# Optimization experiments

Hardware: AMD Instinct MI355X
Metric: run time of the kernel (lower is better)

Reference implementation:

```python
import jax, jax.numpy as jnp
import numpy as np

TEMPERATURE = 0.07
NUM_HARD_NEGATIVES = 5
BATCH, DIM = 4096, 768


def setup_inputs() -> dict:
    key = jax.random.key(0)
    k1, k2 = jax.random.split(key)
    return {
        "text_emb": jax.random.normal(k1, (BATCH, DIM), dtype=jnp.float32),
        "table_emb": jax.random.normal(k2, (BATCH, DIM), dtype=jnp.float32),
    }


def _ttcl_loss(text_emb, table_emb):
    # F.normalize(dim=1)
    t = text_emb / jnp.linalg.norm(text_emb, axis=1, keepdims=True)
    z = table_emb / jnp.linalg.norm(table_emb, axis=1, keepdims=True)
    sim = z @ t.T  # [B, B], sim[i, j] = <table_i, text_j>
    B = sim.shape[0]
    pos = jnp.diagonal(sim) / TEMPERATURE  # [B], <text_i, table_i> == <table_i, text_i>
    diag_mask = jnp.eye(B, dtype=bool)
    neg_inf = jnp.finfo(sim.dtype).min

    def hard_neg_loss(neg_rows):
        # neg_rows[i] holds the B candidate negatives for sample i; exclude self.
        neg = jnp.where(diag_mask, neg_inf, neg_rows)
        top_vals, _ = jax.lax.top_k(neg, NUM_HARD_NEGATIVES)  # [B, k]
        logits = jnp.concatenate([pos[:, None], top_vals / TEMPERATURE], axis=1)  # [B, k+1]
        # cross_entropy with label 0 == -log_softmax(logits)[:, 0]
        return -jax.nn.log_softmax(logits, axis=1)[:, 0]

    # t2z: negatives for i are sim[j][i], j != i  -> column i -> rows of sim.T
    loss_t2z = jnp.sum(hard_neg_loss(sim.T))
    # z2t: negatives for i are sim[i][j], j != i  -> row i
    loss_z2t = jnp.sum(hard_neg_loss(sim))
    loss = (loss_t2z + loss_z2t) / (2 * B)
    return loss, sim


def reference(text_emb, table_emb):
    return _ttcl_loss(text_emb, table_emb)
```

## Files before the change

### kernel.cpp

```cpp
#include <hip/hip_runtime.h>
#include <stdint.h>
#include <math.h>

#define BSZ 4096
#define DIM 768
#define TEMP 0.07f

typedef short short8 __attribute__((ext_vector_type(8)));
typedef float f32x4 __attribute__((ext_vector_type(4)));


__device__ __forceinline__ uint16_t f2bf(float f) {
  uint32_t u = __float_as_uint(f);
  uint32_t r = (u + 0x7FFFu + ((u >> 16) & 1u)) >> 16;
  return (uint16_t)r;
}

__device__ __forceinline__ void gll16(const void* g, void* l) {
  __builtin_amdgcn_global_load_lds(
      (__attribute__((address_space(1))) void*)(uintptr_t)g,
      (__attribute__((address_space(3))) void*)l,
      16, 0, 0);
}

__device__ __forceinline__ void ins5(float v, float& a, float& b, float& c,
                                     float& d, float& e) {
  if (v > e) {
    e = v;
    if (e > d) { float t = d; d = e; e = t;
      if (d > c) { t = c; c = d; d = t;
        if (c > b) { t = b; b = c; c = t;
          if (b > a) { t = a; a = b; b = t; } } } }
  }
}

__device__ __forceinline__ void sins5(float v, float& a, float& b, float& c,
                                      float& d, float& e) {
  float t;
  t = fmaxf(a, v); v = fminf(a, v); a = t;
  t = fmaxf(b, v); v = fminf(b, v); b = t;
  t = fmaxf(c, v); v = fminf(c, v); c = t;
  t = fmaxf(d, v); v = fminf(d, v); d = t;
  e = fmaxf(e, v);
}

__global__ __launch_bounds__(256) void k_norm(const float* __restrict__ text,
                                              const float* __restrict__ table,
                                              uint16_t* __restrict__ tn,
                                              uint16_t* __restrict__ zn) {
  int row = blockIdx.x & (BSZ - 1);
  bool isTable = blockIdx.x >= BSZ;
  const float* src = (isTable ? table : text) + (size_t)row * DIM;
  uint16_t* dst = (isTable ? zn : tn) + (size_t)row * DIM;
  int tid = threadIdx.x;

  float x0 = src[tid];
  float x1 = src[tid + 256];
  float x2 = src[tid + 512];
  float ss = x0 * x0 + x1 * x1 + x2 * x2;
  #pragma unroll
  for (int off = 32; off >= 1; off >>= 1) ss += __shfl_xor(ss, off);
  __shared__ float wss[4];
  if ((tid & 63) == 0) wss[tid >> 6] = ss;
  __syncthreads();
  float inv = rsqrtf(wss[0] + wss[1] + wss[2] + wss[3]);
  dst[tid]       = f2bf(x0 * inv);
  dst[tid + 256] = f2bf(x1 * inv);
  dst[tid + 512] = f2bf(x2 * inv);
}

__global__ __launch_bounds__(512, 2) void k_gemm(const uint16_t* __restrict__ Zb,
                                                 const uint16_t* __restrict__ Tb,
                                                 float* __restrict__ sim) {
  extern __shared__ __attribute__((aligned(16))) char lds[];

  int tid = threadIdx.x;
  int wave = tid >> 6, lane = tid & 63;
  int wm = wave >> 2, wn = wave & 3;
  int brow = (blockIdx.x >> 4) << 8;
  int bcol = (blockIdx.x & 15) << 8;

  f32x4 acc[8][4] = {};

  const uint16_t* gA = Zb + (size_t)brow * DIM;
  const uint16_t* gB = Tb + (size_t)bcol * DIM;

  int r7 = lane & 7;
  int kqg = lane >> 4;
  int rlo = lane & 15;

  int srow = (wave << 5) + (lane >> 3);
  int sc = ((lane & 7) ^ (srow & 7)) << 3;

  auto SA = [&](int t, int bb, int j) {
    gll16(gA + (size_t)(srow + j * 8) * DIM + t * 64 + sc,
          lds + bb + (wave << 12) + (j << 10));
  };
  auto SB = [&](int t, int bb, int j) {
    gll16(gB + (size_t)(srow + j * 8) * DIM + t * 64 + sc,
          lds + bb + 32768 + (wave << 12) + (j << 10));
  };

  auto LOADB = [&](int bb, short8 (&bf)[2][4]) {
    const char* Bb = lds + bb + 32768;
    #pragma unroll
    for (int ks = 0; ks < 2; ++ks) {
      int ch = (((ks << 2) + kqg) ^ r7) << 4;
      #pragma unroll
      for (int n = 0; n < 4; ++n) {
        int R = (wn << 6) + (n << 4) + rlo;
        bf[ks][n] = *(const short8*)(Bb + (R << 7) + ch);
      }
    }
  };
  auto PHASE = [&](int bb, int mlo, short8 (&bf)[2][4]) {
    __builtin_amdgcn_s_setprio(1);
    #pragma unroll
    for (int ks = 0; ks < 2; ++ks) {
      int ch = (((ks << 2) + kqg) ^ r7) << 4;
      #pragma unroll
      for (int mm = 0; mm < 4; ++mm) {
        int R = (wm << 7) + ((mlo + mm) << 4) + rlo;
        short8 af = *(const short8*)(lds + bb + (R << 7) + ch);
        #pragma unroll
        for (int n = 0; n < 4; ++n)
          acc[mlo + mm][n] = __builtin_amdgcn_mfma_f32_16x16x32_bf16(
              af, bf[ks][n], acc[mlo + mm][n], 0, 0, 0);
      }
    }
    __builtin_amdgcn_s_setprio(0);
  };

  #pragma unroll
  for (int j = 0; j < 4; ++j) { SA(0, 0, j); SB(0, 0, j); }
  #pragma unroll
  for (int j = 0; j < 4; ++j) { SA(1, 65536, j); SB(1, 65536, j); }
  asm volatile("s_waitcnt vmcnt(8)" ::: "memory");
  __builtin_amdgcn_s_barrier();

  #pragma unroll 2
  for (int t = 0; t < 10; ++t) {
    int bb = (t & 1) << 16;
    short8 bf[2][4];
    LOADB(bb, bf);
    PHASE(bb, 0, bf);
    __builtin_amdgcn_s_barrier();
    if ((wave & 2) == 0) {
      SA(t + 2, bb, 0); SA(t + 2, bb, 1); SA(t + 2, bb, 2); SA(t + 2, bb, 3);
    }
    SB(t + 2, bb, 0); SB(t + 2, bb, 1);
    SB(t + 2, bb, 2); SB(t + 2, bb, 3);
    PHASE(bb, 4, bf);
    __builtin_amdgcn_s_barrier();
    if ((wave & 2) != 0) {
      SA(t + 2, bb, 0); SA(t + 2, bb, 1); SA(t + 2, bb, 2); SA(t + 2, bb, 3);
    }
    asm volatile("s_waitcnt vmcnt(8)" ::: "memory");
    __builtin_amdgcn_s_barrier();
  }

  {
    short8 bf[2][4];
    LOADB(0, bf);
    PHASE(0, 0, bf);
    PHASE(0, 4, bf);
  }
  asm volatile("s_waitcnt vmcnt(0)" ::: "memory");
  __builtin_amdgcn_s_barrier();
  {
    short8 bf[2][4];
    LOADB(65536, bf);
    PHASE(65536, 0, bf);
    PHASE(65536, 4, bf);
  }

  int crow0 = brow + (wm << 7) + ((lane >> 4) << 2);
  int ccol0 = bcol + (wn << 6) + (lane & 15);
  #pragma unroll
  for (int m = 0; m < 8; ++m)
    #pragma unroll
    for (int n = 0; n < 4; ++n)
      #pragma unroll
      for (int r = 0; r < 4; ++r)
        sim[(size_t)(crow0 + m * 16 + r) * BSZ + (ccol0 + n * 16)] = acc[m][n][r];
}

__global__ __launch_bounds__(256) void k_tile(const float* __restrict__ sim,
                                              float* __restrict__ rp,
                                              float* __restrict__ cp) {
  extern __shared__ float l32[];
  int tid = threadIdx.x;
  int tr = blockIdx.x >> 5, tc = blockIdx.x & 31;
  int row0 = tr << 7, col0 = tc << 7;
  bool diag = (tr == tc);

  int q = tid & 31;
  int g = tid >> 5;
  const float* gsrc = sim + (size_t)(row0 + (g << 4)) * BSZ + col0 + (q << 2);

  f32x4 v[16];
  #pragma unroll
  for (int k = 0; k < 16; ++k)
    v[k] = *(const f32x4*)(gsrc + (size_t)k * BSZ);

  #pragma unroll
  for (int k = 0; k < 16; ++k) {
    int r = (g << 4) + k;
    if (diag && (r >> 2) == q) v[k][r & 3] = -1e30f;
    *(f32x4*)(l32 + (r << 7) + ((q ^ (r & 7)) << 2)) = v[k];
  }
  __syncthreads();

  {
    int row = tid >> 1, h = tid & 1;
    int rx = row & 7;
    const float* rb = l32 + (row << 7);
    float a0 = -1e30f, a1 = -1e30f, a2 = -1e30f, a3 = -1e30f, a4 = -1e30f;
    #pragma unroll
    for (int j = 0; j < 16; ++j) {
      int c16 = (h << 4) + j;
      f32x4 x = *(const f32x4*)(rb + ((c16 ^ rx) << 2));
      sins5(x[0], a0, a1, a2, a3, a4);
      sins5(x[1], a0, a1, a2, a3, a4);
      sins5(x[2], a0, a1, a2, a3, a4);
      sins5(x[3], a0, a1, a2, a3, a4);
    }
    float b0 = __shfl_xor(a0, 1), b1 = __shfl_xor(a1, 1),
          b2 = __shfl_xor(a2, 1), b3 = __shfl_xor(a3, 1),
          b4 = __shfl_xor(a4, 1);
    sins5(b0, a0, a1, a2, a3, a4);
    sins5(b1, a0, a1, a2, a3, a4);
    sins5(b2, a0, a1, a2, a3, a4);
    sins5(b3, a0, a1, a2, a3, a4);
    sins5(b4, a0, a1, a2, a3, a4);
    if (h == 0) {
      float* pr = rp + ((size_t)(row0 + row) * 32 + tc) * 5;
      pr[0] = a0; pr[1] = a1; pr[2] = a2; pr[3] = a3; pr[4] = a4;
    }
  }

  {
    int c = tid >> 1, hf = tid & 1;
    int cc = c >> 2, cw = c & 3;
    float a0 = -1e30f, a1 = -1e30f, a2 = -1e30f, a3 = -1e30f, a4 = -1e30f;
    #pragma unroll 8
    for (int k = 0; k < 64; ++k) {
      int r = (hf << 6) + k;
      float x = l32[(r << 7) + (((cc ^ (r & 7)) << 2) | cw)];
      sins5(x, a0, a1, a2, a3, a4);
    }
    float b0 = __shfl_xor(a0, 1), b1 = __shfl_xor(a1, 1),
          b2 = __shfl_xor(a2, 1), b3 = __shfl_xor(a3, 1),
          b4 = __shfl_xor(a4, 1);
    sins5(b0, a0, a1, a2, a3, a4);
    sins5(b1, a0, a1, a2, a3, a4);
    sins5(b2, a0, a1, a2, a3, a4);
    sins5(b3, a0, a1, a2, a3, a4);
    sins5(b4, a0, a1, a2, a3, a4);
    if (hf == 0) {
      float* pc = cp + ((size_t)(col0 + c) * 32 + tr) * 5;
      pc[0] = a0; pc[1] = a1; pc[2] = a2; pc[3] = a3; pc[4] = a4;
    }
  }
}

__global__ __launch_bounds__(256) void k_merge(const float* __restrict__ sim,
                                               const float* __restrict__ rp,
                                               const float* __restrict__ cp,
                                               float* __restrict__ lossbuf) {
  int wave = threadIdx.x >> 6, lane = threadIdx.x & 63;
  int wid = blockIdx.x * 4 + wave;
  bool isCol = wid >= BSZ;
  int line = isCol ? wid - BSZ : wid;
  const float* src = (isCol ? cp : rp) + (size_t)line * 160;

  float t0 = -1e30f, t1 = -1e30f, t2 = -1e30f, t3 = -1e30f, t4 = -1e30f;
  ins5(src[lane], t0, t1, t2, t3, t4);
  ins5(src[lane + 64], t0, t1, t2, t3, t4);
  if (lane < 32) ins5(src[lane + 128], t0, t1, t2, t3, t4);

  float top[5];
  #pragma unroll
  for (int e = 0; e < 5; e++) {
    float m = t0;
    #pragma unroll
    for (int off = 32; off >= 1; off >>= 1) m = fmaxf(m, __shfl_xor(m, off));
    unsigned long long msk = __ballot(t0 == m);
    int owner = __ffsll(msk) - 1;
    if (lane == owner) { t0 = t1; t1 = t2; t2 = t3; t3 = t4; t4 = -1e30f; }
    top[e] = m;
  }

  if (lane == 0) {
    float pos = sim[(size_t)line * BSZ + line] / TEMP;
    float l0 = top[0] / TEMP, l1 = top[1] / TEMP, l2 = top[2] / TEMP,
          l3 = top[3] / TEMP, l4 = top[4] / TEMP;
    float mx = fmaxf(pos, fmaxf(fmaxf(l0, l1), fmaxf(fmaxf(l2, l3), l4)));
    float s = expf(pos - mx) + expf(l0 - mx) + expf(l1 - mx) +
              expf(l2 - mx) + expf(l3 - mx) + expf(l4 - mx);
    lossbuf[wid] = mx + logf(s) - pos;
  }
}

__global__ __launch_bounds__(256) void k_reduce(const float* __restrict__ losses,
                                                float* __restrict__ out) {
  int tid = threadIdx.x;
  float s = 0.f;
  for (int i = tid; i < 2 * BSZ; i += 256) s += losses[i];
  #pragma unroll
  for (int off = 32; off >= 1; off >>= 1) s += __shfl_xor(s, off);
  __shared__ float wss[4];
  if ((tid & 63) == 0) wss[tid >> 6] = s;
  __syncthreads();
  if (tid == 0) out[0] = (wss[0] + wss[1] + wss[2] + wss[3]) / (2.0f * BSZ);
}

extern "C" void kernel_launch(void* const* d_in, const int* in_sizes, int n_in,
                              void* d_out, int out_size, void* d_ws, size_t ws_size,
                              hipStream_t stream) {
  const float* text = (const float*)d_in[0];
  const float* table = (const float*)d_in[1];
  float* out = (float*)d_out;
  float* sim = out + 1;

  uint16_t* Zb = (uint16_t*)d_ws;
  uint16_t* Tb = Zb + (size_t)BSZ * DIM;
  float* lossbuf = (float*)(Tb + (size_t)BSZ * DIM);

  float* rp = (float*)d_ws;
  float* cp = rp + (size_t)BSZ * 32 * 5;

  k_norm<<<2 * BSZ, 256, 0, stream>>>(text, table, Tb, Zb);
  k_gemm<<<(BSZ / 256) * (BSZ / 256), 512, 131072, stream>>>(Zb, Tb, sim);
  k_tile<<<32 * 32, 256, 65536, stream>>>(sim, rp, cp);
  k_merge<<<2 * BSZ / 4, 256, 0, stream>>>(sim, rp, cp, lossbuf);
  k_reduce<<<1, 256, 0, stream>>>(lossbuf, out);
}
```

Baseline: 84.36 us.

## Vectorize norm kernel and halve top-k tile height with XCD-aware block mapping

The norm kernel now uses 192 threads, each doing one float4 load and one packed 4-bf16 store instead of three scalar accesses. The top-k tile kernel switches to 64x128 tiles with half the shared memory, giving twice as many blocks. Block indices are remapped so that neighbouring column tiles land on the same XCD. Column partials now hold 64 per-tile top-5 entries per column, so the merge kernel reads 320 values on the column path. The aim is better occupancy and cache locality, in exchange for more partial data to merge.

```diff
diff --git a/kernel.cpp b/kernel.cpp
--- a/kernel.cpp
+++ b/kernel.cpp
@@ -7,6 +7,7 @@
 #define TEMP 0.07f
 
 typedef short short8 __attribute__((ext_vector_type(8)));
+typedef short short4v __attribute__((ext_vector_type(4)));
 typedef float f32x4 __attribute__((ext_vector_type(4)));
 
 
@@ -44,7 +45,7 @@
   e = fmaxf(e, v);
 }
 
-__global__ __launch_bounds__(256) void k_norm(const float* __restrict__ text,
+__global__ __launch_bounds__(192) void k_norm(const float* __restrict__ text,
                                               const float* __restrict__ table,
                                               uint16_t* __restrict__ tn,
                                               uint16_t* __restrict__ zn) {
@@ -54,19 +55,20 @@
   uint16_t* dst = (isTable ? zn : tn) + (size_t)row * DIM;
   int tid = threadIdx.x;
 
-  float x0 = src[tid];
-  float x1 = src[tid + 256];
-  float x2 = src[tid + 512];
-  float ss = x0 * x0 + x1 * x1 + x2 * x2;
+  f32x4 v = *(const f32x4*)(src + tid * 4);
+  float ss = v[0] * v[0] + v[1] * v[1] + v[2] * v[2] + v[3] * v[3];
   #pragma unroll
   for (int off = 32; off >= 1; off >>= 1) ss += __shfl_xor(ss, off);
-  __shared__ float wss[4];
+  __shared__ float wss[3];
   if ((tid & 63) == 0) wss[tid >> 6] = ss;
   __syncthreads();
-  float inv = rsqrtf(wss[0] + wss[1] + wss[2] + wss[3]);
-  dst[tid]       = f2bf(x0 * inv);
-  dst[tid + 256] = f2bf(x1 * inv);
-  dst[tid + 512] = f2bf(x2 * inv);
+  float inv = rsqrtf(wss[0] + wss[1] + wss[2]);
+  short4v o;
+  o[0] = (short)f2bf(v[0] * inv);
+  o[1] = (short)f2bf(v[1] * inv);
+  o[2] = (short)f2bf(v[2] * inv);
+  o[3] = (short)f2bf(v[3] * inv);
+  *(short4v*)(dst + tid * 4) = o;
 }
 
 __global__ __launch_bounds__(512, 2) void k_gemm(const uint16_t* __restrict__ Zb,
@@ -190,49 +192,57 @@
                                               float* __restrict__ cp) {
   extern __shared__ float l32[];
   int tid = threadIdx.x;
-  int tr = blockIdx.x >> 5, tc = blockIdx.x & 31;
-  int row0 = tr << 7, col0 = tc << 7;
-  bool diag = (tr == tc);
+
+  int xcd = blockIdx.x & 7, li = blockIdx.x >> 3;
+  int tc = (xcd << 1) + (li & 1) + (((li >> 1) & 1) << 4);
+  int tr = li >> 2;
+  int row0 = tr << 6, col0 = tc << 7;
+  bool diag = ((tr >> 1) == tc);
+  int lcbase = (tr & 1) << 6;
 
   int q = tid & 31;
   int g = tid >> 5;
-  const float* gsrc = sim + (size_t)(row0 + (g << 4)) * BSZ + col0 + (q << 2);
-
-  f32x4 v[16];
-  #pragma unroll
-  for (int k = 0; k < 16; ++k)
+  const float* gsrc = sim + (size_t)(row0 + (g << 3)) * BSZ + col0 + (q << 2);
+
+  f32x4 v[8];
+  #pragma unroll
+  for (int k = 0; k < 8; ++k)
     v[k] = *(const f32x4*)(gsrc + (size_t)k * BSZ);
 
   #pragma unroll
-  for (int k = 0; k < 16; ++k) {
-    int r = (g << 4) + k;
-    if (diag && (r >> 2) == q) v[k][r & 3] = -1e30f;
+  for (int k = 0; k < 8; ++k) {
+    int r = (g << 3) + k;
+    int lc = lcbase + r;
+    if (diag && (lc >> 2) == q) v[k][lc & 3] = -1e30f;
     *(f32x4*)(l32 + (r << 7) + ((q ^ (r & 7)) << 2)) = v[k];
   }
   __syncthreads();
 
   {
-    int row = tid >> 1, h = tid & 1;
+    int row = tid >> 2, h = tid & 3;
     int rx = row & 7;
     const float* rb = l32 + (row << 7);
     float a0 = -1e30f, a1 = -1e30f, a2 = -1e30f, a3 = -1e30f, a4 = -1e30f;
     #pragma unroll
-    for (int j = 0; j < 16; ++j) {
-      int c16 = (h << 4) + j;
+    for (int j = 0; j < 8; ++j) {
+      int c16 = (h << 3) + j;
       f32x4 x = *(const f32x4*)(rb + ((c16 ^ rx) << 2));
       sins5(x[0], a0, a1, a2, a3, a4);
       sins5(x[1], a0, a1, a2, a3, a4);
       sins5(x[2], a0, a1, a2, a3, a4);
       sins5(x[3], a0, a1, a2, a3, a4);
     }
-    float b0 = __shfl_xor(a0, 1), b1 = __shfl_xor(a1, 1),
-          b2 = __shfl_xor(a2, 1), b3 = __shfl_xor(a3, 1),
-          b4 = __shfl_xor(a4, 1);
-    sins5(b0, a0, a1, a2, a3, a4);
-    sins5(b1, a0, a1, a2, a3, a4);
-    sins5(b2, a0, a1, a2, a3, a4);
-    sins5(b3, a0, a1, a2, a3, a4);
-    sins5(b4, a0, a1, a2, a3, a4);
+    #pragma unroll
+    for (int xr = 1; xr <= 2; xr <<= 1) {
+      float b0 = __shfl_xor(a0, xr), b1 = __shfl_xor(a1, xr),
+            b2 = __shfl_xor(a2, xr), b3 = __shfl_xor(a3, xr),
+            b4 = __shfl_xor(a4, xr);
+      sins5(b0, a0, a1, a2, a3, a4);
+      sins5(b1, a0, a1, a2, a3, a4);
+      sins5(b2, a0, a1, a2, a3, a4);
+      sins5(b3, a0, a1, a2, a3, a4);
+      sins5(b4, a0, a1, a2, a3, a4);
+    }
     if (h == 0) {
       float* pr = rp + ((size_t)(row0 + row) * 32 + tc) * 5;
       pr[0] = a0; pr[1] = a1; pr[2] = a2; pr[3] = a3; pr[4] = a4;
@@ -244,8 +254,8 @@
     int cc = c >> 2, cw = c & 3;
     float a0 = -1e30f, a1 = -1e30f, a2 = -1e30f, a3 = -1e30f, a4 = -1e30f;
     #pragma unroll 8
-    for (int k = 0; k < 64; ++k) {
-      int r = (hf << 6) + k;
+    for (int k = 0; k < 32; ++k) {
+      int r = (hf << 5) + k;
       float x = l32[(r << 7) + (((cc ^ (r & 7)) << 2) | cw)];
       sins5(x, a0, a1, a2, a3, a4);
     }
@@ -258,7 +268,7 @@
     sins5(b3, a0, a1, a2, a3, a4);
     sins5(b4, a0, a1, a2, a3, a4);
     if (hf == 0) {
-      float* pc = cp + ((size_t)(col0 + c) * 32 + tr) * 5;
+      float* pc = cp + ((size_t)(col0 + c) * 64 + tr) * 5;
       pc[0] = a0; pc[1] = a1; pc[2] = a2; pc[3] = a3; pc[4] = a4;
     }
   }
@@ -272,12 +282,21 @@
   int wid = blockIdx.x * 4 + wave;
   bool isCol = wid >= BSZ;
   int line = isCol ? wid - BSZ : wid;
-  const float* src = (isCol ? cp : rp) + (size_t)line * 160;
 
   float t0 = -1e30f, t1 = -1e30f, t2 = -1e30f, t3 = -1e30f, t4 = -1e30f;
-  ins5(src[lane], t0, t1, t2, t3, t4);
-  ins5(src[lane + 64], t0, t1, t2, t3, t4);
-  if (lane < 32) ins5(src[lane + 128], t0, t1, t2, t3, t4);
+  if (isCol) {
+    const float* src = cp + (size_t)line * 320;
+    ins5(src[lane], t0, t1, t2, t3, t4);
+    ins5(src[lane + 64], t0, t1, t2, t3, t4);
+    ins5(src[lane + 128], t0, t1, t2, t3, t4);
+    ins5(src[lane + 192], t0, t1, t2, t3, t4);
+    ins5(src[lane + 256], t0, t1, t2, t3, t4);
+  } else {
+    const float* src = rp + (size_t)line * 160;
+    ins5(src[lane], t0, t1, t2, t3, t4);
+    ins5(src[lane + 64], t0, t1, t2, t3, t4);
+    if (lane < 32) ins5(src[lane + 128], t0, t1, t2, t3, t4);
+  }
 
   float top[5];
   #pragma unroll
@@ -330,9 +349,9 @@
   float* rp = (float*)d_ws;
   float* cp = rp + (size_t)BSZ * 32 * 5;
 
-  k_norm<<<2 * BSZ, 256, 0, stream>>>(text, table, Tb, Zb);
+  k_norm<<<2 * BSZ, 192, 0, stream>>>(text, table, Tb, Zb);
   k_gemm<<<(BSZ / 256) * (BSZ / 256), 512, 131072, stream>>>(Zb, Tb, sim);
-  k_tile<<<32 * 32, 256, 65536, stream>>>(sim, rp, cp);
+  k_tile<<<(BSZ / 64) * (BSZ / 128), 256, 32768, stream>>>(sim, rp, cp);
   k_merge<<<2 * BSZ / 4, 256, 0, stream>>>(sim, rp, cp, lossbuf);
   k_reduce<<<1, 256, 0, stream>>>(lossbuf, out);
 }
```

New measurement: 81.93 us. 1.03x faster.
